# Kernel optimization log

Measured on AMD Instinct MI355X. Metric: run time of the kernel, lower is better.

The kernel has to match this reference:

```python
import jax, jax.numpy as jnp
import numpy as np

MAX_CACHE_LEN = 1024
B, S, D, H = 8, 512, 512, 8
DK = D // H


def setup_inputs() -> dict:
    key = jax.random.key(0)
    ks = jax.random.split(key, 11)
    w = lambda k: jax.random.normal(k, (D, D), jnp.float32) * 0.02
    b = lambda k: jax.random.normal(k, (D,), jnp.float32) * 0.02
    return {
        "x": jax.random.normal(ks[0], (B, S, D), jnp.float32),
        "prev_k": jax.random.normal(ks[1], (B, H, MAX_CACHE_LEN, DK), jnp.float32),
        "prev_v": jax.random.normal(ks[2], (B, H, MAX_CACHE_LEN, DK), jnp.float32),
        "Wq": w(ks[3]), "bq": b(ks[4]),
        "Wk": w(ks[5]), "bk": b(ks[6]),
        "Wv": w(ks[7]), "bv": b(ks[8]),
        "Wo": w(ks[9]), "bo": b(ks[10]),
        "offset": MAX_CACHE_LEN,  # cache already full (steady-state streaming)
    }


def reference(x, prev_k, prev_v, Wq, bq, Wk, bk, Wv, bv, Wo, bo, offset):
    Bx, Sx, Dx = x.shape
    Hx = prev_k.shape[1]
    dk = Dx // Hx
    # projections (torch Linear: y = x @ W.T + b), split into heads -> [B,H,S,dk]
    def proj(W, bias):
        return (x @ W.T + bias).reshape(Bx, Sx, Hx, dk).transpose(0, 2, 1, 3)
    q = proj(Wq, bq)
    k = jnp.concatenate([prev_k, proj(Wk, bk)], axis=2)
    v = jnp.concatenate([prev_v, proj(Wv, bv)], axis=2)
    # sliding-window narrow to last MAX_CACHE_LEN keys (static shapes under jit)
    k_full = k.shape[2]
    start = max(0, k_full - MAX_CACHE_LEN)
    k = k[:, :, start:, :]
    v = v[:, :, start:, :]
    k_len = k.shape[2]
    new_offset = min(offset + Sx, MAX_CACHE_LEN)
    # scores [B,H,S,k_len]
    scores = jnp.einsum("bhqd,bhkd->bhqk", q, k) * (dk ** -0.5)
    q_start = new_offset - Sx
    q_idx = jnp.arange(Sx)[:, None] + q_start
    k_idx = jnp.arange(k_len)[None, :]
    mask = q_idx < k_idx  # future keys masked
    scores = jnp.where(mask[None, None], -jnp.inf, scores)
    attn = jax.nn.softmax(scores, axis=-1)
    out = jnp.einsum("bhqk,bhkd->bhqd", attn, v)
    out = out.transpose(0, 2, 1, 3).reshape(Bx, Sx, Dx)
    out = out @ Wo.T + bo
    return out, k, v, jnp.asarray(new_offset, jnp.int64 if jax.config.x64_enabled else jnp.int32)
```

## Files before the change

kernel.cpp:

```cpp
#include <hip/hip_runtime.h>
#include <hip/hip_bf16.h>
#include <math.h>

#define B_  8
#define S_  512
#define D_  512
#define H_  8
#define DK_ 64
#define KL_ 1024

typedef __attribute__((ext_vector_type(8))) short bf16x8;
typedef __attribute__((ext_vector_type(4))) float f32x4;

__device__ __forceinline__ unsigned short f2bf(float f) {
    __hip_bfloat16 h = __float2bfloat16(f);
    unsigned short u;
    __builtin_memcpy(&u, &h, 2);
    return u;
}
__device__ __forceinline__ void gld16(const void* g, void* l) {
    __builtin_amdgcn_global_load_lds(
        (const __attribute__((address_space(1))) unsigned int*)g,
        (__attribute__((address_space(3))) unsigned int*)l, 16, 0, 0);
}

__global__ __launch_bounds__(256)
void prep_kernel(const float* __restrict__ x,
                 const float* __restrict__ Wq, const float* __restrict__ Wk,
                 const float* __restrict__ Wv, const float* __restrict__ Wo,
                 unsigned short* __restrict__ xb,
                 unsigned short* __restrict__ Wqb, unsigned short* __restrict__ Wkb,
                 unsigned short* __restrict__ Wvb, unsigned short* __restrict__ Wob,
                 float* __restrict__ off_out) {
    const int blk = blockIdx.x, t = threadIdx.x;
    if (blk == 0 && t == 0) off_out[0] = 1024.0f;

    const float* src; unsigned short* dst; int off;
    if (blk < 1024) {
        src = x; dst = xb; off = blk * 256 + t;
    } else {
        int widx = blk - 1024;
        int grp = widx >> 7, wb = widx & 127;
        const float* ws_[4]        = {Wq, Wk, Wv, Wo};
        unsigned short* wd_[4]     = {Wqb, Wkb, Wvb, Wob};
        src = ws_[grp]; dst = wd_[grp]; off = wb * 256 + t;
    }
    float4 v0 = ((const float4*)src)[off * 2];
    float4 v1 = ((const float4*)src)[off * 2 + 1];
    unsigned short tmp[8] = {f2bf(v0.x), f2bf(v0.y), f2bf(v0.z), f2bf(v0.w),
                             f2bf(v1.x), f2bf(v1.y), f2bf(v1.z), f2bf(v1.w)};
    *(uint4*)&dst[off * 8] = *(uint4*)tmp;
}

__device__ __forceinline__
void prev_copy_body(const float* __restrict__ pk, const float* __restrict__ pv,
                    float* __restrict__ kout, float* __restrict__ vout,
                    unsigned short* __restrict__ Kp, unsigned short* __restrict__ Vp,
                    unsigned char* __restrict__ smem, int pb) {
    float (*Kl)[68] = (float (*)[68])smem;
    float (*Vl)[68] = (float (*)[68])(smem + 17408);
    const int t = threadIdx.x;
    const int kt = pb & 7, bh = pb >> 3;
    const float* Kg = pk + (bh * KL_ + 512 + kt * 64) * DK_;
    const float* Vg = pv + (bh * KL_ + 512 + kt * 64) * DK_;
    float* Ko = kout + (bh * KL_ + kt * 64) * DK_;
    float* Vo = vout + (bh * KL_ + kt * 64) * DK_;
    #pragma unroll
    for (int it = 0; it < 4; ++it) {
        int idx = t + it * 256;
        int row = idx >> 4, c4 = idx & 15;
        float4 kv = *(const float4*)&Kg[row * 64 + c4 * 4];
        float4 vv = *(const float4*)&Vg[row * 64 + c4 * 4];
        *(float4*)&Ko[row * 64 + c4 * 4] = kv;
        *(float4*)&Vo[row * 64 + c4 * 4] = vv;
        *(float4*)&Kl[row][c4 * 4] = kv;
        *(float4*)&Vl[row][c4 * 4] = vv;
    }
    __syncthreads();
    unsigned short* Kpb = Kp + (bh * 16 + kt) * 4096;
    unsigned short* Vpb = Vp + (bh * 16 + kt) * 4096;
    #pragma unroll
    for (int s = 0; s < 2; ++s) {
        int slot = t + s * 256;
        int c = slot >> 6, l = slot & 63;
        int nn = c >> 1, hf = c & 1;
        {
            int row = nn * 16 + (l & 15), col = hf * 32 + (l >> 4) * 8;
            unsigned short tmp[8];
            #pragma unroll
            for (int j = 0; j < 8; ++j) tmp[j] = f2bf(Kl[row][col + j]);
            *(uint4*)&Kpb[c * 512 + l * 8] = *(uint4*)tmp;
        }
        {
            int row0 = hf * 32 + (l >> 4) * 8, col = nn * 16 + (l & 15);
            unsigned short tmp[8];
            #pragma unroll
            for (int j = 0; j < 8; ++j) tmp[j] = f2bf(Vl[row0 + j][col]);
            *(uint4*)&Vpb[c * 512 + l * 8] = *(uint4*)tmp;
        }
    }
    __syncthreads();
}

template<int MODE, int BM>
__device__ __forceinline__
void mfma_gemm_body(const unsigned short* __restrict__ A,
                    const unsigned short* __restrict__ Wb,
                    const float* __restrict__ bias,
                    float* __restrict__ C32, unsigned short* __restrict__ C16,
                    unsigned short* __restrict__ Pk,
                    unsigned char* __restrict__ smem) {
    constexpr int MM = BM / 32;
    constexpr int ABUF = BM * 64;
    const int t = threadIdx.x, l = t & 63, w = t >> 6;
    const int m16 = l & 15, quad = l >> 4;
    const int wm = w >> 1, wn = w & 1;
    const int bn = blockIdx.x, bm = blockIdx.y;
    const int lr = l >> 2, lc = (l & 3) * 8;

    f32x4 acc[MM][2] = {};
    const unsigned short* Ag = A + (bm * BM) * 512;
    const unsigned short* Wg = Wb + (bn * 64) * 512;

    auto stage = [&](int buf, int k0) {
        unsigned short* Asb = (unsigned short*)(smem + buf * ABUF);
        unsigned short* Bsb = (unsigned short*)(smem + 2 * ABUF + buf * 4096);
        #pragma unroll
        for (int q = 0; q < BM / 64; ++q) {
            int chunk = w * (BM / 64) + q;
            gld16(Ag + (chunk * 16 + lr) * 512 + k0 + lc, &Asb[chunk * 512 + l * 8]);
        }
        gld16(Wg + (w * 16 + lr) * 512 + k0 + lc, &Bsb[w * 512 + l * 8]);
    };

    stage(0, 0);
    __syncthreads();
    int buf = 0;
    for (int it = 0; it < 16; ++it) {
        if (it < 15) stage(buf ^ 1, (it + 1) * 32);

        const unsigned short* Asb = (const unsigned short*)(smem + buf * ABUF);
        const unsigned short* Bsb = (const unsigned short*)(smem + 2 * ABUF + buf * 4096);
        bf16x8 af[MM], bfr[2];
        #pragma unroll
        for (int mm = 0; mm < MM; ++mm)
            af[mm] = *(const bf16x8*)&Asb[(wm * (BM / 2) + mm * 16 + m16) * 32 + quad * 8];
        #pragma unroll
        for (int nn = 0; nn < 2; ++nn)
            bfr[nn] = *(const bf16x8*)&Bsb[(wn * 32 + nn * 16 + m16) * 32 + quad * 8];
        #pragma unroll
        for (int mm = 0; mm < MM; ++mm)
            #pragma unroll
            for (int nn = 0; nn < 2; ++nn)
                acc[mm][nn] = __builtin_amdgcn_mfma_f32_16x16x32_bf16(
                    af[mm], bfr[nn], acc[mm][nn], 0, 0, 0);

        __syncthreads();
        buf ^= 1;
    }

    if constexpr (MODE == 2 || MODE == 4) {
        unsigned short* Ts = (unsigned short*)smem;
        #pragma unroll
        for (int mm = 0; mm < MM; ++mm)
            #pragma unroll
            for (int nn = 0; nn < 2; ++nn) {
                int n = bn * 64 + wn * 32 + nn * 16 + m16;
                float bv_ = bias[n];
                int d = n & 63;
                #pragma unroll
                for (int r = 0; r < 4; ++r) {
                    int ml = wm * (BM / 2) + mm * 16 + quad * 4 + r;
                    int m = bm * BM + ml;
                    float val = acc[mm][nn][r] + bv_;
                    int b = m >> 9, s = m & 511, h = n >> 6;
                    C32[((b * H_ + h) * KL_ + 512 + s) * DK_ + d] = val;
                    if (MODE == 2) Ts[ml * 72 + d]  = f2bf(val);
                    else           Ts[d * 136 + ml] = f2bf(val);
                }
            }
        __syncthreads();
        const int bh = (bm >> 2) * H_ + bn;
        const int kt0 = 8 + (bm & 3) * 2;
        #pragma unroll
        for (int T = 0; T < 2; ++T)
            #pragma unroll
            for (int cp = 0; cp < 2; ++cp) {
                int c = w * 2 + cp, nn = c >> 1, hf = c & 1;
                uint4 frag;
                if (MODE == 2)
                    frag = *(const uint4*)&Ts[(T * 64 + nn * 16 + (l & 15)) * 72
                                              + hf * 32 + (l >> 4) * 8];
                else
                    frag = *(const uint4*)&Ts[(nn * 16 + (l & 15)) * 136
                                              + T * 64 + hf * 32 + (l >> 4) * 8];
                *(uint4*)&Pk[((bh * 16 + kt0 + T) * 4096) + c * 512 + l * 8] = frag;
            }
    } else {
        #pragma unroll
        for (int mm = 0; mm < MM; ++mm)
            #pragma unroll
            for (int nn = 0; nn < 2; ++nn) {
                int n = bn * 64 + wn * 32 + nn * 16 + m16;
                float bv_ = bias[n];
                #pragma unroll
                for (int r = 0; r < 4; ++r) {
                    int m = bm * BM + wm * (BM / 2) + mm * 16 + quad * 4 + r;
                    float val = acc[mm][nn][r] + bv_;
                    if (MODE == 3) {
                        C32[m * 512 + n] = val;
                    } else {
                        int b = m >> 9, s = m & 511;
                        int h = n >> 6, d = n & 63;
                        C16[((b * H_ + h) * S_ + s) * DK_ + d] =
                            f2bf(val * 0.18033688011112042f);
                    }
                }
            }
    }
}

__global__ __launch_bounds__(256, 4)
void qkv_mfma_kernel(const unsigned short* __restrict__ xb,
                     const unsigned short* __restrict__ Wqb, const float* __restrict__ bq,
                     const unsigned short* __restrict__ Wkb, const float* __restrict__ bk,
                     const unsigned short* __restrict__ Wvb, const float* __restrict__ bv,
                     unsigned short* __restrict__ Qb, float* __restrict__ kout,
                     float* __restrict__ vout,
                     unsigned short* __restrict__ Kp, unsigned short* __restrict__ Vp,
                     const float* __restrict__ pk, const float* __restrict__ pv) {
    __shared__ __attribute__((aligned(16))) unsigned char smem[34816];
    if (blockIdx.z == 0) {
        int pb0 = blockIdx.y * 8 + blockIdx.x;
        prev_copy_body(pk, pv, kout, vout, Kp, Vp, smem, pb0);
        prev_copy_body(pk, pv, kout, vout, Kp, Vp, smem, pb0 + 256);
    }
    else if (blockIdx.z == 1) mfma_gemm_body<1, 128>(xb, Wqb, bq, nullptr, Qb, nullptr, smem);
    else if (blockIdx.z == 2) mfma_gemm_body<2, 128>(xb, Wkb, bk, kout, nullptr, Kp, smem);
    else                      mfma_gemm_body<4, 128>(xb, Wvb, bv, vout, nullptr, Vp, smem);
}

__global__ __launch_bounds__(256, 4)
void out_mfma_kernel(const unsigned short* __restrict__ Ob, const unsigned short* __restrict__ Wob,
                     const float* __restrict__ bo, float* __restrict__ C) {
    __shared__ __attribute__((aligned(16))) unsigned char smem[16384];
    mfma_gemm_body<3, 64>(Ob, Wob, bo, C, nullptr, nullptr, smem);
}

__global__ __launch_bounds__(128)
void attn_kernel(const unsigned short* __restrict__ Qb,
                 const unsigned short* __restrict__ Kp,
                 const unsigned short* __restrict__ Vp,
                 unsigned short* __restrict__ Ob) {
    const int bh = blockIdx.x, qg = blockIdx.y;
    const int t = threadIdx.x, l = t & 63, w = t >> 6;
    const int m16 = l & 15, quad = l >> 4;
    const int q0 = qg * 32;

    __shared__ __attribute__((aligned(16))) unsigned short Ps[2][32][72];
    __shared__ float comb[64][40];

    bf16x8 qf[2][2];
    #pragma unroll
    for (int qh = 0; qh < 2; ++qh)
        #pragma unroll
        for (int p = 0; p < 2; ++p)
            qf[qh][p] = *(const bf16x8*)(Qb + (bh * S_ + q0 + qh * 16 + m16) * DK_
                                            + p * 32 + quad * 8);

    f32x4 acc[2][4] = {};
    float psum[2][4] = {};

    const int ktmax = (543 + q0) >> 6;
    const unsigned short* Kpb = Kp + (bh * 16) * 4096;
    const unsigned short* Vpb = Vp + (bh * 16) * 4096;

    for (int kt = w; kt <= ktmax; kt += 2) {
        const unsigned short* kb = Kpb + kt * 4096;
        const unsigned short* vb = Vpb + kt * 4096;
        bf16x8 kf[4][2];
        #pragma unroll
        for (int nn = 0; nn < 4; ++nn)
            #pragma unroll
            for (int hf = 0; hf < 2; ++hf)
                kf[nn][hf] = *(const bf16x8*)(kb + ((nn * 2 + hf) * 64 + l) * 8);

        f32x4 sc[2][4];
        __builtin_amdgcn_s_setprio(1);
        #pragma unroll
        for (int qh = 0; qh < 2; ++qh)
            #pragma unroll
            for (int nn = 0; nn < 4; ++nn) {
                sc[qh][nn][0] = sc[qh][nn][1] = sc[qh][nn][2] = sc[qh][nn][3] = 0.f;
                sc[qh][nn] = __builtin_amdgcn_mfma_f32_16x16x32_bf16(qf[qh][0], kf[nn][0], sc[qh][nn], 0, 0, 0);
                sc[qh][nn] = __builtin_amdgcn_mfma_f32_16x16x32_bf16(qf[qh][1], kf[nn][1], sc[qh][nn], 0, 0, 0);
            }
        __builtin_amdgcn_s_setprio(0);

        bf16x8 vf[4][2];
        #pragma unroll
        for (int nn = 0; nn < 4; ++nn)
            #pragma unroll
            for (int hf = 0; hf < 2; ++hf)
                vf[nn][hf] = *(const bf16x8*)(vb + ((nn * 2 + hf) * 64 + l) * 8);

        if (kt == ktmax) {
            #pragma unroll
            for (int qh = 0; qh < 2; ++qh)
                #pragma unroll
                for (int nn = 0; nn < 4; ++nn) {
                    int key = kt * 64 + nn * 16 + m16;
                    #pragma unroll
                    for (int r = 0; r < 4; ++r)
                        if (key > 512 + q0 + qh * 16 + (quad << 2) + r)
                            sc[qh][nn][r] = -INFINITY;
                }
        }

        #pragma unroll
        for (int qh = 0; qh < 2; ++qh)
            #pragma unroll
            for (int nn = 0; nn < 4; ++nn)
                #pragma unroll
                for (int r = 0; r < 4; ++r) {
                    float p = exp2f(sc[qh][nn][r]);
                    psum[qh][r] += p;
                    Ps[w][qh * 16 + (quad << 2) + r][nn * 16 + m16] = f2bf(p);
                }

        bf16x8 pf[2][2];
        #pragma unroll
        for (int qh = 0; qh < 2; ++qh)
            #pragma unroll
            for (int hf = 0; hf < 2; ++hf)
                pf[qh][hf] = *(const bf16x8*)&Ps[w][qh * 16 + m16][hf * 32 + quad * 8];
        __builtin_amdgcn_s_setprio(1);
        #pragma unroll
        for (int qh = 0; qh < 2; ++qh)
            #pragma unroll
            for (int nn = 0; nn < 4; ++nn) {
                acc[qh][nn] = __builtin_amdgcn_mfma_f32_16x16x32_bf16(pf[qh][0], vf[nn][0], acc[qh][nn], 0, 0, 0);
                acc[qh][nn] = __builtin_amdgcn_mfma_f32_16x16x32_bf16(pf[qh][1], vf[nn][1], acc[qh][nn], 0, 0, 0);
            }
        __builtin_amdgcn_s_setprio(0);
    }

    if (w == 0) {
        #pragma unroll
        for (int qh = 0; qh < 2; ++qh)
            #pragma unroll
            for (int nn = 0; nn < 4; ++nn)
                #pragma unroll
                for (int r = 0; r < 4; ++r)
                    comb[l][(qh * 4 + nn) * 4 + r] = acc[qh][nn][r];
        #pragma unroll
        for (int qh = 0; qh < 2; ++qh)
            #pragma unroll
            for (int r = 0; r < 4; ++r)
                comb[l][32 + qh * 4 + r] = psum[qh][r];
    }
    __syncthreads();
    if (w == 1) {
        #pragma unroll
        for (int qh = 0; qh < 2; ++qh)
            #pragma unroll
            for (int nn = 0; nn < 4; ++nn)
                #pragma unroll
                for (int r = 0; r < 4; ++r)
                    acc[qh][nn][r] += comb[l][(qh * 4 + nn) * 4 + r];
        float inv[2][4];
        #pragma unroll
        for (int qh = 0; qh < 2; ++qh)
            #pragma unroll
            for (int r = 0; r < 4; ++r) {
                float ps = psum[qh][r] + comb[l][32 + qh * 4 + r];
                ps += __shfl_xor(ps, 1);
                ps += __shfl_xor(ps, 2);
                ps += __shfl_xor(ps, 4);
                ps += __shfl_xor(ps, 8);
                inv[qh][r] = 1.f / ps;
            }
        unsigned short* Og = Ob + ((bh >> 3) * S_ + q0) * D_ + (bh & 7) * DK_;
        #pragma unroll
        for (int qh = 0; qh < 2; ++qh)
            #pragma unroll
            for (int r = 0; r < 4; ++r)
                #pragma unroll
                for (int nn = 0; nn < 4; ++nn)
                    Og[(qh * 16 + (quad << 2) + r) * D_ + nn * 16 + m16] =
                        f2bf(acc[qh][nn][r] * inv[qh][r]);
    }
}

extern "C" void kernel_launch(void* const* d_in, const int* in_sizes, int n_in,
                              void* d_out, int out_size, void* d_ws, size_t ws_size,
                              hipStream_t stream) {
    const float* x  = (const float*)d_in[0];
    const float* pk = (const float*)d_in[1];
    const float* pv = (const float*)d_in[2];
    const float* Wq = (const float*)d_in[3];
    const float* bq = (const float*)d_in[4];
    const float* Wk = (const float*)d_in[5];
    const float* bk = (const float*)d_in[6];
    const float* Wv = (const float*)d_in[7];
    const float* bv = (const float*)d_in[8];
    const float* Wo = (const float*)d_in[9];
    const float* bo = (const float*)d_in[10];

    float* out     = (float*)d_out;
    float* kout    = out + 2097152;
    float* vout    = kout + 4194304;
    float* off_out = vout + 4194304;

    unsigned short* xb  = (unsigned short*)d_ws;
    unsigned short* Wqb = xb + 2097152;
    unsigned short* Wkb = Wqb + 262144;
    unsigned short* Wvb = Wkb + 262144;
    unsigned short* Wob = Wvb + 262144;
    unsigned short* Qb  = Wob + 262144;
    unsigned short* Kp  = Qb + 2097152;
    unsigned short* Vp  = Kp + 4194304;
    unsigned short* Ob  = xb;

    prep_kernel<<<1536, 256, 0, stream>>>(x, Wq, Wk, Wv, Wo,
                                          xb, Wqb, Wkb, Wvb, Wob, off_out);
    qkv_mfma_kernel<<<dim3(8, 32, 4), 256, 0, stream>>>(xb, Wqb, bq, Wkb, bk, Wvb, bv,
                                                        Qb, kout, vout, Kp, Vp, pk, pv);
    attn_kernel<<<dim3(64, 16), 128, 0, stream>>>(Qb, Kp, Vp, Ob);
    out_mfma_kernel<<<dim3(8, 64), 256, 0, stream>>>(Ob, Wob, bo, out);
}
```

Baseline: 155.0 us.

## Fuse fp32-to-bf16 conversion into QKV GEMM loads and drop prep kernel

Removes the separate prep kernel that converted x and all weights to bf16. The QKV GEMM now loads fp32 tiles into registers, converts them to bf16 and writes them to LDS, with the load prefetch overlapped against the MFMA work. Wo conversion and the offset write move into the prev-copy blocks. This saves a launch and a full fp32 read plus bf16 write-and-reread of x, at the cost of extra fp32 traffic per GEMM tile (x is re-read by 8 column blocks across 3 projections), higher register use (launch bounds dropped to 3 waves), and loss of the async global_load_lds path.

```diff
diff --git a/kernel.cpp b/kernel.cpp
--- a/kernel.cpp
+++ b/kernel.cpp
@@ -22,34 +22,6 @@
     __builtin_amdgcn_global_load_lds(
         (const __attribute__((address_space(1))) unsigned int*)g,
         (__attribute__((address_space(3))) unsigned int*)l, 16, 0, 0);
-}
-
-__global__ __launch_bounds__(256)
-void prep_kernel(const float* __restrict__ x,
-                 const float* __restrict__ Wq, const float* __restrict__ Wk,
-                 const float* __restrict__ Wv, const float* __restrict__ Wo,
-                 unsigned short* __restrict__ xb,
-                 unsigned short* __restrict__ Wqb, unsigned short* __restrict__ Wkb,
-                 unsigned short* __restrict__ Wvb, unsigned short* __restrict__ Wob,
-                 float* __restrict__ off_out) {
-    const int blk = blockIdx.x, t = threadIdx.x;
-    if (blk == 0 && t == 0) off_out[0] = 1024.0f;
-
-    const float* src; unsigned short* dst; int off;
-    if (blk < 1024) {
-        src = x; dst = xb; off = blk * 256 + t;
-    } else {
-        int widx = blk - 1024;
-        int grp = widx >> 7, wb = widx & 127;
-        const float* ws_[4]        = {Wq, Wk, Wv, Wo};
-        unsigned short* wd_[4]     = {Wqb, Wkb, Wvb, Wob};
-        src = ws_[grp]; dst = wd_[grp]; off = wb * 256 + t;
-    }
-    float4 v0 = ((const float4*)src)[off * 2];
-    float4 v1 = ((const float4*)src)[off * 2 + 1];
-    unsigned short tmp[8] = {f2bf(v0.x), f2bf(v0.y), f2bf(v0.z), f2bf(v0.w),
-                             f2bf(v1.x), f2bf(v1.y), f2bf(v1.z), f2bf(v1.w)};
-    *(uint4*)&dst[off * 8] = *(uint4*)tmp;
 }
 
 __device__ __forceinline__
@@ -102,10 +74,11 @@
     __syncthreads();
 }
 
-template<int MODE, int BM>
+template<int MODE, int BM, bool CONV>
 __device__ __forceinline__
 void mfma_gemm_body(const unsigned short* __restrict__ A,
                     const unsigned short* __restrict__ Wb,
+                    const float* __restrict__ A32, const float* __restrict__ W32,
                     const float* __restrict__ bias,
                     float* __restrict__ C32, unsigned short* __restrict__ C16,
                     unsigned short* __restrict__ Pk,
@@ -119,8 +92,17 @@
     const int lr = l >> 2, lc = (l & 3) * 8;
 
     f32x4 acc[MM][2] = {};
-    const unsigned short* Ag = A + (bm * BM) * 512;
-    const unsigned short* Wg = Wb + (bn * 64) * 512;
+    const unsigned short* Ag = nullptr;
+    const unsigned short* Wg = nullptr;
+    const float* Ag32 = nullptr;
+    const float* Wg32 = nullptr;
+    if constexpr (CONV) {
+        Ag32 = A32 + (bm * BM) * 512;
+        Wg32 = W32 + (bn * 64) * 512;
+    } else {
+        Ag = A + (bm * BM) * 512;
+        Wg = Wb + (bn * 64) * 512;
+    }
 
     auto stage = [&](int buf, int k0) {
         unsigned short* Asb = (unsigned short*)(smem + buf * ABUF);
@@ -133,11 +115,49 @@
         gld16(Wg + (w * 16 + lr) * 512 + k0 + lc, &Bsb[w * 512 + l * 8]);
     };
 
-    stage(0, 0);
+    float4 ra[6];
+    auto load_regs = [&](int k0) {
+        if constexpr (CONV) {
+            #pragma unroll
+            for (int i = 0; i < 2; ++i) {
+                int s = t + i * 256;
+                int row = s >> 2, c8 = (s & 3) * 8;
+                ra[i * 2 + 0] = *(const float4*)&Ag32[row * 512 + k0 + c8];
+                ra[i * 2 + 1] = *(const float4*)&Ag32[row * 512 + k0 + c8 + 4];
+            }
+            int row = t >> 2, c8 = (t & 3) * 8;
+            ra[4] = *(const float4*)&Wg32[row * 512 + k0 + c8];
+            ra[5] = *(const float4*)&Wg32[row * 512 + k0 + c8 + 4];
+        }
+    };
+    auto write_lds = [&](int buf) {
+        if constexpr (CONV) {
+            unsigned short* Asb = (unsigned short*)(smem + buf * ABUF);
+            unsigned short* Bsb = (unsigned short*)(smem + 2 * ABUF + buf * 4096);
+            #pragma unroll
+            for (int i = 0; i < 2; ++i) {
+                int s = t + i * 256;
+                unsigned short tmp[8] = {
+                    f2bf(ra[i * 2].x), f2bf(ra[i * 2].y), f2bf(ra[i * 2].z), f2bf(ra[i * 2].w),
+                    f2bf(ra[i * 2 + 1].x), f2bf(ra[i * 2 + 1].y), f2bf(ra[i * 2 + 1].z), f2bf(ra[i * 2 + 1].w)};
+                *(uint4*)&Asb[s * 8] = *(uint4*)tmp;
+            }
+            unsigned short tmp[8] = {
+                f2bf(ra[4].x), f2bf(ra[4].y), f2bf(ra[4].z), f2bf(ra[4].w),
+                f2bf(ra[5].x), f2bf(ra[5].y), f2bf(ra[5].z), f2bf(ra[5].w)};
+            *(uint4*)&Bsb[t * 8] = *(uint4*)tmp;
+        }
+    };
+
+    if constexpr (CONV) { load_regs(0); write_lds(0); }
+    else                { stage(0, 0); }
     __syncthreads();
     int buf = 0;
     for (int it = 0; it < 16; ++it) {
-        if (it < 15) stage(buf ^ 1, (it + 1) * 32);
+        if (it < 15) {
+            if constexpr (CONV) load_regs((it + 1) * 32);
+            else                stage(buf ^ 1, (it + 1) * 32);
+        }
 
         const unsigned short* Asb = (const unsigned short*)(smem + buf * ABUF);
         const unsigned short* Bsb = (const unsigned short*)(smem + 2 * ABUF + buf * 4096);
@@ -155,6 +175,7 @@
                 acc[mm][nn] = __builtin_amdgcn_mfma_f32_16x16x32_bf16(
                     af[mm], bfr[nn], acc[mm][nn], 0, 0, 0);
 
+        if constexpr (CONV) { if (it < 15) write_lds(buf ^ 1); }
         __syncthreads();
         buf ^= 1;
     }
@@ -220,31 +241,43 @@
     }
 }
 
-__global__ __launch_bounds__(256, 4)
-void qkv_mfma_kernel(const unsigned short* __restrict__ xb,
-                     const unsigned short* __restrict__ Wqb, const float* __restrict__ bq,
-                     const unsigned short* __restrict__ Wkb, const float* __restrict__ bk,
-                     const unsigned short* __restrict__ Wvb, const float* __restrict__ bv,
+__global__ __launch_bounds__(256, 3)
+void qkv_mfma_kernel(const float* __restrict__ x,
+                     const float* __restrict__ Wq, const float* __restrict__ bq,
+                     const float* __restrict__ Wk, const float* __restrict__ bk,
+                     const float* __restrict__ Wv, const float* __restrict__ bv,
+                     const float* __restrict__ Wo, unsigned short* __restrict__ Wob,
                      unsigned short* __restrict__ Qb, float* __restrict__ kout,
                      float* __restrict__ vout,
                      unsigned short* __restrict__ Kp, unsigned short* __restrict__ Vp,
-                     const float* __restrict__ pk, const float* __restrict__ pv) {
+                     const float* __restrict__ pk, const float* __restrict__ pv,
+                     float* __restrict__ off_out) {
     __shared__ __attribute__((aligned(16))) unsigned char smem[34816];
     if (blockIdx.z == 0) {
         int pb0 = blockIdx.y * 8 + blockIdx.x;
+        if (pb0 == 0 && threadIdx.x == 0) off_out[0] = 1024.0f;
+        {
+            int base = pb0 * 1024 + threadIdx.x * 4;
+            float4 wv = *(const float4*)&Wo[base];
+            unsigned short tmp[4] = {f2bf(wv.x), f2bf(wv.y), f2bf(wv.z), f2bf(wv.w)};
+            *(uint2*)&Wob[base] = *(uint2*)tmp;
+        }
         prev_copy_body(pk, pv, kout, vout, Kp, Vp, smem, pb0);
         prev_copy_body(pk, pv, kout, vout, Kp, Vp, smem, pb0 + 256);
     }
-    else if (blockIdx.z == 1) mfma_gemm_body<1, 128>(xb, Wqb, bq, nullptr, Qb, nullptr, smem);
-    else if (blockIdx.z == 2) mfma_gemm_body<2, 128>(xb, Wkb, bk, kout, nullptr, Kp, smem);
-    else                      mfma_gemm_body<4, 128>(xb, Wvb, bv, vout, nullptr, Vp, smem);
+    else if (blockIdx.z == 1)
+        mfma_gemm_body<1, 128, true>(nullptr, nullptr, x, Wq, bq, nullptr, Qb, nullptr, smem);
+    else if (blockIdx.z == 2)
+        mfma_gemm_body<2, 128, true>(nullptr, nullptr, x, Wk, bk, kout, nullptr, Kp, smem);
+    else
+        mfma_gemm_body<4, 128, true>(nullptr, nullptr, x, Wv, bv, vout, nullptr, Vp, smem);
 }
 
 __global__ __launch_bounds__(256, 4)
 void out_mfma_kernel(const unsigned short* __restrict__ Ob, const unsigned short* __restrict__ Wob,
                      const float* __restrict__ bo, float* __restrict__ C) {
     __shared__ __attribute__((aligned(16))) unsigned char smem[16384];
-    mfma_gemm_body<3, 64>(Ob, Wob, bo, C, nullptr, nullptr, smem);
+    mfma_gemm_body<3, 64, false>(Ob, Wob, nullptr, nullptr, bo, C, nullptr, nullptr, smem);
 }
 
 __global__ __launch_bounds__(128)
@@ -412,20 +445,15 @@
     float* vout    = kout + 4194304;
     float* off_out = vout + 4194304;
 
-    unsigned short* xb  = (unsigned short*)d_ws;
-    unsigned short* Wqb = xb + 2097152;
-    unsigned short* Wkb = Wqb + 262144;
-    unsigned short* Wvb = Wkb + 262144;
-    unsigned short* Wob = Wvb + 262144;
+    unsigned short* Ob  = (unsigned short*)d_ws;
+    unsigned short* Wob = Ob + 2097152;
     unsigned short* Qb  = Wob + 262144;
     unsigned short* Kp  = Qb + 2097152;
     unsigned short* Vp  = Kp + 4194304;
-    unsigned short* Ob  = xb;
-
-    prep_kernel<<<1536, 256, 0, stream>>>(x, Wq, Wk, Wv, Wo,
-                                          xb, Wqb, Wkb, Wvb, Wob, off_out);
-    qkv_mfma_kernel<<<dim3(8, 32, 4), 256, 0, stream>>>(xb, Wqb, bq, Wkb, bk, Wvb, bv,
-                                                        Qb, kout, vout, Kp, Vp, pk, pv);
+
+    qkv_mfma_kernel<<<dim3(8, 32, 4), 256, 0, stream>>>(x, Wq, bq, Wk, bk, Wv, bv,
+                                                        Wo, Wob, Qb, kout, vout,
+                                                        Kp, Vp, pk, pv, off_out);
     attn_kernel<<<dim3(64, 16), 128, 0, stream>>>(Qb, Kp, Vp, Ob);
     out_mfma_kernel<<<dim3(8, 64), 256, 0, stream>>>(Ob, Wob, bo, out);
 }
```

Result: no change. 156.9 us (+1.2%).
